# Optimization experiments

Measured on AMD Instinct MI355X. Metric: run time of the kernel, lower is better.

Reference implementation:

```python
import jax, jax.numpy as jnp
import numpy as np

HID = 512
ALPHA = 0.01
PI = np.float32(np.pi)


def _mlp(x, W0, b0, W1, b1, W2, b2, W3, b3):
    # x: [..., 2] -> scalar field u(x): [...]
    h = jnp.tanh(x @ W0 + b0)
    h = jnp.tanh(h @ W1 + b1)
    h = jnp.tanh(h @ W2 + b2)
    return (h @ W3 + b3)[..., 0]


def _forcing(x):
    # f = -Delta u for u = sin(pi x) sin(pi y^2)
    xx, yy = x[:, 0], x[:, 1]
    return (-PI ** 2 * (1 + 4 * yy ** 2) * jnp.sin(PI * xx) * jnp.sin(PI * yy ** 2)
            + 2 * PI * jnp.sin(PI * xx) * jnp.cos(PI * yy ** 2))


def setup_inputs() -> dict:
    key = jax.random.key(0)
    ks = jax.random.split(key, 6)
    n_i, n_b = 20000, 800
    x_interior = jax.random.uniform(ks[0], (n_i, 2), dtype=jnp.float32)  # domain (0,1)
    theta = jnp.linspace(0.0, 2.0 * np.pi, n_b)
    x_boundary = jnp.stack([(jnp.cos(theta) + 1.0) * 0.5,
                            (jnp.sin(theta) + 1.0) * 0.5], axis=1).astype(jnp.float32)

    def w(k, shape, fan_in):
        return (jax.random.normal(k, shape, jnp.float32) / np.float32(np.sqrt(fan_in)))

    W0 = w(ks[1], (2, HID), 2)
    b0 = jnp.zeros((HID,), jnp.float32)
    W1 = w(ks[2], (HID, HID), HID)
    b1 = jnp.zeros((HID,), jnp.float32)
    W2 = w(ks[3], (HID, HID), HID)
    b2 = jnp.zeros((HID,), jnp.float32)
    W3 = w(ks[4], (HID, 1), HID)
    b3 = jnp.zeros((1,), jnp.float32)
    return dict(x_interior=x_interior, x_boundary=x_boundary,
                W0=W0, b0=b0, W1=W1, b1=b1, W2=W2, b2=b2, W3=W3, b3=b3)


def reference(x_interior, x_boundary, W0, b0, W1, b1, W2, b2, W3, b3):
    params = (W0, b0, W1, b1, W2, b2, W3, b3)

    def u_scalar(x):  # x: [2] -> scalar
        return _mlp(x, *params)

    g = jax.grad(u_scalar)

    def lap_one(x):
        # Laplacian = trace of Hessian via forward-over-reverse HVPs
        lap = jnp.float32(0.0)
        for i in range(2):
            e = jnp.zeros((2,), x.dtype).at[i].set(1.0)
            _, hv = jax.jvp(g, (x,), (e,))
            lap = lap + hv[i]
        return lap

    laplacian = jax.vmap(lap_one)(x_interior)  # [n_interior]
    interior_loss = jnp.mean((laplacian - _forcing(x_interior)) ** 2)
    boundary_loss = jnp.mean(_mlp(x_boundary, *params) ** 2)
    total_loss = ALPHA * interior_loss + boundary_loss
    return total_loss, interior_loss, boundary_loss
```

## Files before the change

kernel.cpp:

```cpp
#include <hip/hip_runtime.h>
#include <math.h>

#define HID 512
#define KP 520
#define PPB 16

typedef __attribute__((ext_vector_type(8))) _Float16 half8;
typedef __attribute__((ext_vector_type(4))) _Float16 half4;
typedef __attribute__((ext_vector_type(4))) float f32x4;

static __device__ __forceinline__ float fast_tanh(float x) {
    float e = __expf(2.f * x);
    return 1.f - 2.f / (e + 1.f);
}

__global__ __launch_bounds__(256) void prep_wt(
    const float* __restrict__ W1, const float* __restrict__ W2,
    _Float16* __restrict__ W1h, _Float16* __restrict__ W2h)
{
    int b = blockIdx.x;
    const float* W = (b < 1024) ? W1 : W2;
    _Float16* Wh   = (b < 1024) ? W1h : W2h;
    int gid = (b & 1023) * 256 + threadIdx.x;
    int k8   = gid & 7;
    int quad = (gid >> 3) & 3;
    int l15  = (gid >> 5) & 15;
    int kb   = (gid >> 9) & 15;
    int jb   = gid >> 13;
    int j = jb * 16 + l15;
    int k = kb * 32 + quad * 8 + k8;
    Wh[gid] = (_Float16)W[k * HID + j];
}

template<bool FULL>
static __device__ __forceinline__ void layer_pass(
    const _Float16* __restrict__ Wh, const float* __restrict__ bias,
    _Float16 (*Als)[PPB][KP], int wv, int lane)
{
    const int l15 = lane & 15, quad = lane >> 4;
    const int j0w = wv * 128;
    const int jb0 = wv * 8;
    const int foff = l15 * 32 + quad * 8;

    f32x4 acc[4][8];
    #pragma unroll
    for (int s = 0; s < 4; ++s)
        #pragma unroll
        for (int jt = 0; jt < 8; ++jt) acc[s][jt] = (f32x4)0.f;

    half8 wA[8], wB[8];
    #pragma unroll
    for (int jt = 0; jt < 8; ++jt)
        wA[jt] = *(const half8*)(Wh + (size_t)((jb0 + jt) * 16) * 512 + foff);

    auto iter = [&](int kb, half8 (&wc)[8], half8 (&wn)[8]) {
        half8 a[4];
        #pragma unroll
        for (int s = 0; s < 4; ++s)
            a[s] = *(const half8*)&Als[s][l15][kb * 32 + quad * 8];
        if (kb < 15) {
            #pragma unroll
            for (int jt = 0; jt < 8; ++jt)
                wn[jt] = *(const half8*)(Wh + (size_t)((jb0 + jt) * 16 + kb + 1) * 512 + foff);
        }
        #pragma unroll
        for (int s = 0; s < 4; ++s)
            #pragma unroll
            for (int jt = 0; jt < 8; ++jt)
                acc[s][jt] = __builtin_amdgcn_mfma_f32_16x16x32_f16(
                    wc[jt], a[s], acc[s][jt], 0, 0, 0);
    };

    #pragma unroll
    for (int kb = 0; kb < 16; kb += 2) {
        iter(kb,     wA, wB);
        iter(kb + 1, wB, wA);
    }

    __syncthreads();

    #pragma unroll
    for (int jt = 0; jt < 8; ++jt) {
        const int jbase = j0w + jt * 16 + quad * 4;
        f32x4 bv = *(const f32x4*)&bias[jbase];
        half4 vh, vt1, vt2, vS;
        #pragma unroll
        for (int r = 0; r < 4; ++r) {
            float a  = fast_tanh(acc[0][jt][r] + bv[r]);
            float g  = 1.f - a * a;
            float z1 = acc[1][jt][r];
            float z2 = acc[2][jt][r];
            vh[r] = (_Float16)a;
            if (FULL) {
                vt1[r] = (_Float16)(g * z1);
                vt2[r] = (_Float16)(g * z2);
            }
            vS[r] = (_Float16)(g * acc[3][jt][r] - 2.f * a * g * (z1 * z1 + z2 * z2));
        }
        *(half4*)&Als[0][l15][jbase] = vh;
        if (FULL) {
            *(half4*)&Als[1][l15][jbase] = vt1;
            *(half4*)&Als[2][l15][jbase] = vt2;
        }
        *(half4*)&Als[3][l15][jbase] = vS;
    }
    __syncthreads();
}

__global__ __launch_bounds__(256, 2) void pois_fused(
    const float* __restrict__ x_int, const float* __restrict__ x_bnd,
    const float* __restrict__ W0, const float* __restrict__ b0,
    const _Float16* __restrict__ W1h, const float* __restrict__ b1,
    const _Float16* __restrict__ W2h, const float* __restrict__ b2,
    const float* __restrict__ W3, const float* __restrict__ b3,
    float* __restrict__ partials, int NI, int NT, int nblk)
{
    __shared__ _Float16 Als[4][PPB][KP];
    __shared__ float sc[32];

    const int tid = threadIdx.x;
    const int wv = tid >> 6, lane = tid & 63;
    const int p0 = blockIdx.x * PPB;

    {
        const int p = tid & 15, kc = tid >> 4;
        int gp = p0 + p;
        int gpc = (gp >= NT) ? 0 : gp;
        float xx, yy;
        if (gpc < NI) { xx = x_int[2 * gpc];        yy = x_int[2 * gpc + 1]; }
        else          { xx = x_bnd[2 * (gpc - NI)]; yy = x_bnd[2 * (gpc - NI) + 1]; }
        #pragma unroll
        for (int k8 = 0; k8 < 4; ++k8) {
            const int k = kc * 32 + k8 * 8;
            f32x4 w0a = *(const f32x4*)&W0[k],       w0b = *(const f32x4*)&W0[k + 4];
            f32x4 w1a = *(const f32x4*)&W0[HID + k], w1b = *(const f32x4*)&W0[HID + k + 4];
            f32x4 b0a = *(const f32x4*)&b0[k],       b0b = *(const f32x4*)&b0[k + 4];
            half8 vh, vt1, vt2, vS;
            #pragma unroll
            for (int i = 0; i < 8; ++i) {
                float w0i = (i < 4) ? w0a[i] : w0b[i - 4];
                float w1i = (i < 4) ? w1a[i] : w1b[i - 4];
                float bbi = (i < 4) ? b0a[i] : b0b[i - 4];
                float a = fast_tanh(xx * w0i + yy * w1i + bbi);
                float g = 1.f - a * a;
                vh[i]  = (_Float16)a;
                vt1[i] = (_Float16)(g * w0i);
                vt2[i] = (_Float16)(g * w1i);
                vS[i]  = (_Float16)(-2.f * a * g * (w0i * w0i + w1i * w1i));
            }
            *(half8*)&Als[0][p][k] = vh;
            *(half8*)&Als[1][p][k] = vt1;
            *(half8*)&Als[2][p][k] = vt2;
            *(half8*)&Als[3][p][k] = vS;
        }
    }
    __syncthreads();

    layer_pass<true >(W1h, b1, Als, wv, lane);
    layer_pass<false>(W2h, b2, Als, wv, lane);

    {
        const int psub = lane >> 4, kc = lane & 15;
        const int p = wv * 4 + psub;
        float u = 0.f, lap = 0.f;
        #pragma unroll
        for (int k8 = 0; k8 < 4; ++k8) {
            const int k = kc * 32 + k8 * 8;
            half8 hh = *(const half8*)&Als[0][p][k];
            half8 ss = *(const half8*)&Als[3][p][k];
            f32x4 wa = *(const f32x4*)&W3[k], wb = *(const f32x4*)&W3[k + 4];
            #pragma unroll
            for (int i = 0; i < 8; ++i) {
                float w = (i < 4) ? wa[i] : wb[i - 4];
                u   += (float)hh[i] * w;
                lap += (float)ss[i] * w;
            }
        }
        #pragma unroll
        for (int off = 1; off < 16; off <<= 1) {
            u   += __shfl_xor(u, off);
            lap += __shfl_xor(lap, off);
        }
        if (kc == 0) {
            int gp = p0 + p;
            float vi = 0.f, vb = 0.f;
            if (gp < NI) {
                const float PIf = 3.14159265358979323846f;
                float xx = x_int[2 * gp], yy = x_int[2 * gp + 1];
                float sx = sinf(PIf * xx);
                float y2 = yy * yy;
                float sy = sinf(PIf * y2), cy = cosf(PIf * y2);
                float f = -PIf * PIf * (1.f + 4.f * y2) * sx * sy + 2.f * PIf * sx * cy;
                float r = lap - f;
                vi = r * r;
            } else if (gp < NT) {
                float uu = u + b3[0];
                vb = uu * uu;
            }
            sc[p * 2] = vi; sc[p * 2 + 1] = vb;
        }
    }
    __syncthreads();
    if (tid == 0) {
        float svi = 0.f, svb = 0.f;
        #pragma unroll
        for (int p = 0; p < PPB; ++p) { svi += sc[p * 2]; svb += sc[p * 2 + 1]; }
        partials[blockIdx.x] = svi;
        partials[nblk + blockIdx.x] = svb;
    }
}

__global__ __launch_bounds__(256) void pois_reduce(
    const float* __restrict__ partials, float* __restrict__ out,
    int nblk, int NI, int NB)
{
    int tid = threadIdx.x;
    float si = 0.f, sb = 0.f;
    for (int i = tid; i < nblk; i += 256) {
        si += partials[i];
        sb += partials[nblk + i];
    }
    #pragma unroll
    for (int off = 32; off > 0; off >>= 1) {
        si += __shfl_xor(si, off);
        sb += __shfl_xor(sb, off);
    }
    __shared__ float ri[4], rb[4];
    int wv = tid >> 6;
    if ((tid & 63) == 0) { ri[wv] = si; rb[wv] = sb; }
    __syncthreads();
    if (tid == 0) {
        float inter = (ri[0] + ri[1] + ri[2] + ri[3]) / (float)NI;
        float bound = (rb[0] + rb[1] + rb[2] + rb[3]) / (float)NB;
        out[0] = 0.01f * inter + bound;
        out[1] = inter;
        out[2] = bound;
    }
}

extern "C" void kernel_launch(void* const* d_in, const int* in_sizes, int n_in,
                              void* d_out, int out_size, void* d_ws, size_t ws_size,
                              hipStream_t stream)
{
    const float* x_int = (const float*)d_in[0];
    const float* x_bnd = (const float*)d_in[1];
    const float* W0 = (const float*)d_in[2];
    const float* b0 = (const float*)d_in[3];
    const float* W1 = (const float*)d_in[4];
    const float* b1 = (const float*)d_in[5];
    const float* W2 = (const float*)d_in[6];
    const float* b2 = (const float*)d_in[7];
    const float* W3 = (const float*)d_in[8];
    const float* b3 = (const float*)d_in[9];

    int NI = in_sizes[0] / 2;
    int NB = in_sizes[1] / 2;
    int NT = NI + NB;
    int nblk = (NT + PPB - 1) / PPB;

    float* partials = (float*)d_ws;
    _Float16* W1h = (_Float16*)((char*)d_ws + 16384);
    _Float16* W2h = W1h + 262144;

    prep_wt<<<2048, 256, 0, stream>>>(W1, W2, W1h, W2h);

    pois_fused<<<nblk, 256, 0, stream>>>(
        x_int, x_bnd, W0, b0, W1h, b1, W2h, b2, W3, b3,
        partials, NI, NT, nblk);

    pois_reduce<<<1, 256, 0, stream>>>(partials, (float*)d_out, nblk, NI, NB);
}
```

Before: 205.9 us.

## Use 8-wave blocks with slab LDS layout and tiled weight transpose

The fused kernel now runs 512 threads per block, so each wave owns 64 output columns instead of 128, halving per-wave accumulator registers and aiming at more waves per CU. Activations in LDS move to a k-block slab layout matching the MFMA fragment order, and the final dot product is reorganized for 32-lane reductions. The weight prep kernel now transposes through a padded shared tile for coalesced reads. The trade-off is that each weight fragment is now reused across fewer output columns per wave, and 512-thread blocks are coarser to schedule.

New measurement: 193.7 us. 1.06x faster.

```diff
diff --git a/kernel.cpp b/kernel.cpp
--- a/kernel.cpp
+++ b/kernel.cpp
@@ -2,8 +2,8 @@
 #include <math.h>
 
 #define HID 512
-#define KP 520
 #define PPB 16
+#define SLAB 512
 
 typedef __attribute__((ext_vector_type(8))) _Float16 half8;
 typedef __attribute__((ext_vector_type(4))) _Float16 half4;
@@ -18,55 +18,69 @@
     const float* __restrict__ W1, const float* __restrict__ W2,
     _Float16* __restrict__ W1h, _Float16* __restrict__ W2h)
 {
+    __shared__ float T[64][65];
     int b = blockIdx.x;
-    const float* W = (b < 1024) ? W1 : W2;
-    _Float16* Wh   = (b < 1024) ? W1h : W2h;
-    int gid = (b & 1023) * 256 + threadIdx.x;
-    int k8   = gid & 7;
-    int quad = (gid >> 3) & 3;
-    int l15  = (gid >> 5) & 15;
-    int kb   = (gid >> 9) & 15;
-    int jb   = gid >> 13;
-    int j = jb * 16 + l15;
-    int k = kb * 32 + quad * 8 + k8;
-    Wh[gid] = (_Float16)W[k * HID + j];
+    const float* W = (b < 64) ? W1 : W2;
+    _Float16* Wh   = (b < 64) ? W1h : W2h;
+    int tb = b & 63;
+    int jbG = tb >> 3, kbG = tb & 7;
+    int j0 = jbG * 64, k0 = kbG * 64;
+    int t = threadIdx.x;
+    #pragma unroll
+    for (int r = 0; r < 16; ++r) {
+        int kl = r * 4 + (t >> 6);
+        int jl = t & 63;
+        T[kl][jl] = W[(size_t)(k0 + kl) * HID + j0 + jl];
+    }
+    __syncthreads();
+    int ljb = t >> 6, l15 = (t >> 2) & 15, quad = t & 3;
+    #pragma unroll
+    for (int lkb = 0; lkb < 2; ++lkb) {
+        half8 v;
+        #pragma unroll
+        for (int k8 = 0; k8 < 8; ++k8)
+            v[k8] = (_Float16)T[lkb * 32 + quad * 8 + k8][ljb * 16 + l15];
+        size_t out = (size_t)((jbG * 4 + ljb) * 16 + (kbG * 2 + lkb)) * SLAB
+                   + l15 * 32 + quad * 8;
+        *(half8*)(Wh + out) = v;
+    }
 }
 
 template<bool FULL>
 static __device__ __forceinline__ void layer_pass(
     const _Float16* __restrict__ Wh, const float* __restrict__ bias,
-    _Float16 (*Als)[PPB][KP], int wv, int lane)
+    _Float16* Als, int wv, int lane)
 {
     const int l15 = lane & 15, quad = lane >> 4;
-    const int j0w = wv * 128;
-    const int jb0 = wv * 8;
-    const int foff = l15 * 32 + quad * 8;
-
-    f32x4 acc[4][8];
+    const int j0w = wv * 64;
+    const int jb0 = wv * 4;
+    const int loff = l15 * 32 + quad * 8;
+
+    f32x4 acc[4][4];
     #pragma unroll
     for (int s = 0; s < 4; ++s)
         #pragma unroll
-        for (int jt = 0; jt < 8; ++jt) acc[s][jt] = (f32x4)0.f;
-
-    half8 wA[8], wB[8];
-    #pragma unroll
-    for (int jt = 0; jt < 8; ++jt)
-        wA[jt] = *(const half8*)(Wh + (size_t)((jb0 + jt) * 16) * 512 + foff);
-
-    auto iter = [&](int kb, half8 (&wc)[8], half8 (&wn)[8]) {
+        for (int jt = 0; jt < 4; ++jt) acc[s][jt] = (f32x4)0.f;
+
+    half8 wA[4], wB[4];
+    #pragma unroll
+    for (int jt = 0; jt < 4; ++jt)
+        wA[jt] = *(const half8*)(Wh + (size_t)((jb0 + jt) * 16) * SLAB + loff);
+
+    auto iter = [&](int kb, half8 (&wc)[4], half8 (&wn)[4]) {
         half8 a[4];
         #pragma unroll
         for (int s = 0; s < 4; ++s)
-            a[s] = *(const half8*)&Als[s][l15][kb * 32 + quad * 8];
+            a[s] = *(const half8*)(Als + (s * 16 + kb) * SLAB + loff);
         if (kb < 15) {
             #pragma unroll
-            for (int jt = 0; jt < 8; ++jt)
-                wn[jt] = *(const half8*)(Wh + (size_t)((jb0 + jt) * 16 + kb + 1) * 512 + foff);
+            for (int jt = 0; jt < 4; ++jt)
+                wn[jt] = *(const half8*)(Wh + (size_t)((jb0 + jt) * 16 + kb + 1) * SLAB + loff);
         }
         #pragma unroll
         for (int s = 0; s < 4; ++s)
             #pragma unroll
-            for (int jt = 0; jt < 8; ++jt)
+            for (int jt = 0; jt < 4; ++jt)
                 acc[s][jt] = __builtin_amdgcn_mfma_f32_16x16x32_f16(
                     wc[jt], a[s], acc[s][jt], 0, 0, 0);
     };
@@ -80,7 +94,7 @@
     __syncthreads();
 
     #pragma unroll
-    for (int jt = 0; jt < 8; ++jt) {
+    for (int jt = 0; jt < 4; ++jt) {
         const int jbase = j0w + jt * 16 + quad * 4;
         f32x4 bv = *(const f32x4*)&bias[jbase];
         half4 vh, vt1, vt2, vS;
@@ -97,17 +111,19 @@
             }
             vS[r] = (_Float16)(g * acc[3][jt][r] - 2.f * a * g * (z1 * z1 + z2 * z2));
         }
-        *(half4*)&Als[0][l15][jbase] = vh;
+        const int okb = jbase >> 5;
+        const int ooff = l15 * 32 + (jbase & 31);
+        *(half4*)(Als + (0 * 16 + okb) * SLAB + ooff) = vh;
         if (FULL) {
-            *(half4*)&Als[1][l15][jbase] = vt1;
-            *(half4*)&Als[2][l15][jbase] = vt2;
-        }
-        *(half4*)&Als[3][l15][jbase] = vS;
-    }
-    __syncthreads();
-}
-
-__global__ __launch_bounds__(256, 2) void pois_fused(
+            *(half4*)(Als + (1 * 16 + okb) * SLAB + ooff) = vt1;
+            *(half4*)(Als + (2 * 16 + okb) * SLAB + ooff) = vt2;
+        }
+        *(half4*)(Als + (3 * 16 + okb) * SLAB + ooff) = vS;
+    }
+    __syncthreads();
+}
+
+__global__ __launch_bounds__(512, 4) void pois_fused(
     const float* __restrict__ x_int, const float* __restrict__ x_bnd,
     const float* __restrict__ W0, const float* __restrict__ b0,
     const _Float16* __restrict__ W1h, const float* __restrict__ b1,
@@ -115,7 +131,7 @@
     const float* __restrict__ W3, const float* __restrict__ b3,
     float* __restrict__ partials, int NI, int NT, int nblk)
 {
-    __shared__ _Float16 Als[4][PPB][KP];
+    __shared__ _Float16 Als[4 * 16 * SLAB];
     __shared__ float sc[32];
 
     const int tid = threadIdx.x;
@@ -123,35 +139,37 @@
     const int p0 = blockIdx.x * PPB;
 
     {
-        const int p = tid & 15, kc = tid >> 4;
+        const int p = lane >> 2, quad = lane & 3;
         int gp = p0 + p;
         int gpc = (gp >= NT) ? 0 : gp;
         float xx, yy;
         if (gpc < NI) { xx = x_int[2 * gpc];        yy = x_int[2 * gpc + 1]; }
         else          { xx = x_bnd[2 * (gpc - NI)]; yy = x_bnd[2 * (gpc - NI) + 1]; }
         #pragma unroll
-        for (int k8 = 0; k8 < 4; ++k8) {
-            const int k = kc * 32 + k8 * 8;
+        for (int i = 0; i < 2; ++i) {
+            const int kb = wv * 2 + i;
+            const int k = kb * 32 + quad * 8;
             f32x4 w0a = *(const f32x4*)&W0[k],       w0b = *(const f32x4*)&W0[k + 4];
             f32x4 w1a = *(const f32x4*)&W0[HID + k], w1b = *(const f32x4*)&W0[HID + k + 4];
             f32x4 b0a = *(const f32x4*)&b0[k],       b0b = *(const f32x4*)&b0[k + 4];
             half8 vh, vt1, vt2, vS;
             #pragma unroll
-            for (int i = 0; i < 8; ++i) {
-                float w0i = (i < 4) ? w0a[i] : w0b[i - 4];
-                float w1i = (i < 4) ? w1a[i] : w1b[i - 4];
-                float bbi = (i < 4) ? b0a[i] : b0b[i - 4];
+            for (int e = 0; e < 8; ++e) {
+                float w0i = (e < 4) ? w0a[e] : w0b[e - 4];
+                float w1i = (e < 4) ? w1a[e] : w1b[e - 4];
+                float bbi = (e < 4) ? b0a[e] : b0b[e - 4];
                 float a = fast_tanh(xx * w0i + yy * w1i + bbi);
                 float g = 1.f - a * a;
-                vh[i]  = (_Float16)a;
-                vt1[i] = (_Float16)(g * w0i);
-                vt2[i] = (_Float16)(g * w1i);
-                vS[i]  = (_Float16)(-2.f * a * g * (w0i * w0i + w1i * w1i));
+                vh[e]  = (_Float16)a;
+                vt1[e] = (_Float16)(g * w0i);
+                vt2[e] = (_Float16)(g * w1i);
+                vS[e]  = (_Float16)(-2.f * a * g * (w0i * w0i + w1i * w1i));
             }
-            *(half8*)&Als[0][p][k] = vh;
-            *(half8*)&Als[1][p][k] = vt1;
-            *(half8*)&Als[2][p][k] = vt2;
-            *(half8*)&Als[3][p][k] = vS;
+            const int off = p * 32 + quad * 8;
+            *(half8*)(Als + (0 * 16 + kb) * SLAB + off) = vh;
+            *(half8*)(Als + (1 * 16 + kb) * SLAB + off) = vt1;
+            *(half8*)(Als + (2 * 16 + kb) * SLAB + off) = vt2;
+            *(half8*)(Als + (3 * 16 + kb) * SLAB + off) = vS;
         }
     }
     __syncthreads();
@@ -160,28 +178,31 @@
     layer_pass<false>(W2h, b2, Als, wv, lane);
 
     {
-        const int psub = lane >> 4, kc = lane & 15;
-        const int p = wv * 4 + psub;
+        const int hl = lane >> 5, l5 = lane & 31;
+        const int p = wv * 2 + hl;
+        const int kb = l5 >> 1;
+        const int off = p * 32 + (l5 & 1) * 16;
+        half8 h0 = *(const half8*)(Als + (0 * 16 + kb) * SLAB + off);
+        half8 h1 = *(const half8*)(Als + (0 * 16 + kb) * SLAB + off + 8);
+        half8 s0 = *(const half8*)(Als + (3 * 16 + kb) * SLAB + off);
+        half8 s1 = *(const half8*)(Als + (3 * 16 + kb) * SLAB + off + 8);
+        const int k0 = l5 * 16;
+        f32x4 wa = *(const f32x4*)&W3[k0],     wb = *(const f32x4*)&W3[k0 + 4];
+        f32x4 wc = *(const f32x4*)&W3[k0 + 8], wd = *(const f32x4*)&W3[k0 + 12];
         float u = 0.f, lap = 0.f;
         #pragma unroll
-        for (int k8 = 0; k8 < 4; ++k8) {
-            const int k = kc * 32 + k8 * 8;
-            half8 hh = *(const half8*)&Als[0][p][k];
-            half8 ss = *(const half8*)&Als[3][p][k];
-            f32x4 wa = *(const f32x4*)&W3[k], wb = *(const f32x4*)&W3[k + 4];
-            #pragma unroll
-            for (int i = 0; i < 8; ++i) {
-                float w = (i < 4) ? wa[i] : wb[i - 4];
-                u   += (float)hh[i] * w;
-                lap += (float)ss[i] * w;
-            }
-        }
-        #pragma unroll
-        for (int off = 1; off < 16; off <<= 1) {
-            u   += __shfl_xor(u, off);
-            lap += __shfl_xor(lap, off);
-        }
-        if (kc == 0) {
+        for (int e = 0; e < 4; ++e) {
+            u   += (float)h0[e] * wa[e] + (float)h0[e + 4] * wb[e]
+                 + (float)h1[e] * wc[e] + (float)h1[e + 4] * wd[e];
+            lap += (float)s0[e] * wa[e] + (float)s0[e + 4] * wb[e]
+                 + (float)s1[e] * wc[e] + (float)s1[e + 4] * wd[e];
+        }
+        #pragma unroll
+        for (int off2 = 1; off2 < 32; off2 <<= 1) {
+            u   += __shfl_xor(u, off2);
+            lap += __shfl_xor(lap, off2);
+        }
+        if (l5 == 0) {
             int gp = p0 + p;
             float vi = 0.f, vb = 0.f;
             if (gp < NI) {
@@ -262,9 +283,9 @@
     _Float16* W1h = (_Float16*)((char*)d_ws + 16384);
     _Float16* W2h = W1h + 262144;
 
-    prep_wt<<<2048, 256, 0, stream>>>(W1, W2, W1h, W2h);
-
-    pois_fused<<<nblk, 256, 0, stream>>>(
+    prep_wt<<<128, 256, 0, stream>>>(W1, W2, W1h, W2h);
+
+    pois_fused<<<nblk, 512, 0, stream>>>(
         x_int, x_bnd, W0, b0, W1h, b1, W2h, b2, W3, b3,
         partials, NI, NT, nblk);
 
```
